# Optimization experiments

Hardware: AMD Instinct MI355X
Metric: run time of the kernel (lower is better)

Reference implementation:

```python
import jax, jax.numpy as jnp
import numpy as np

N_NODES = 100000
IN_DIM = 64
HID = 128
HID2 = HID // 2
N_CLASSES = 2
N_EDGES = 1600000
BN_EPS = 1e-5


def setup_inputs() -> dict:
    key = jax.random.key(0)
    ks = jax.random.split(key, 12)
    x = jax.random.normal(ks[0], (N_NODES, IN_DIM), dtype=jnp.float32)
    edge_index = jax.random.randint(ks[1], (2, N_EDGES), 0, N_NODES, dtype=jnp.int64)
    s = lambda k, shp, fan: jax.random.normal(k, shp, dtype=jnp.float32) / np.sqrt(fan)
    return {
        "x": x,
        "edge_index": edge_index,
        # SAGEConv1: lin_l (on aggregated neighbors, has bias), lin_r (root, no bias)
        "W1_l": s(ks[2], (IN_DIM, HID), IN_DIM),
        "b1_l": jnp.zeros((HID,), jnp.float32),
        "W1_r": s(ks[3], (IN_DIM, HID), IN_DIM),
        # SAGEConv2
        "W2_l": s(ks[4], (HID, HID2), HID),
        "b2_l": jnp.zeros((HID2,), jnp.float32),
        "W2_r": s(ks[5], (HID, HID2), HID),
        # BatchNorm (eval mode: running stats)
        "bn1_gamma": jnp.ones((HID,), jnp.float32),
        "bn1_beta": jnp.zeros((HID,), jnp.float32),
        "bn1_mean": jax.random.normal(ks[6], (HID,), dtype=jnp.float32) * 0.1,
        "bn1_var": jax.random.uniform(ks[7], (HID,), minval=0.5, maxval=1.5, dtype=jnp.float32),
        "bn2_gamma": jnp.ones((HID2,), jnp.float32),
        "bn2_beta": jnp.zeros((HID2,), jnp.float32),
        "bn2_mean": jax.random.normal(ks[8], (HID2,), dtype=jnp.float32) * 0.1,
        "bn2_var": jax.random.uniform(ks[9], (HID2,), minval=0.5, maxval=1.5, dtype=jnp.float32),
        # classifier
        "Wc": s(ks[10], (HID2, N_CLASSES), HID2),
        "bc": jnp.zeros((N_CLASSES,), jnp.float32),
    }


def _sage_mean(h, src, dst, Wl, bl, Wr, n_nodes):
    # gather source-node features along edges, scatter-mean into destinations
    msg = h[src]                                            # [E, D]
    summed = jax.ops.segment_sum(msg, dst, num_segments=n_nodes)  # [N, D]
    cnt = jax.ops.segment_sum(jnp.ones_like(dst, dtype=h.dtype), dst, num_segments=n_nodes)
    mean = summed / jnp.maximum(cnt, 1.0)[:, None]
    return mean @ Wl + bl + h @ Wr


def _bn_eval(h, gamma, beta, mean, var):
    return (h - mean) * (gamma * jax.lax.rsqrt(var + BN_EPS)) + beta


def reference(x, edge_index, W1_l, b1_l, W1_r, W2_l, b2_l, W2_r,
              bn1_gamma, bn1_beta, bn1_mean, bn1_var,
              bn2_gamma, bn2_beta, bn2_mean, bn2_var, Wc, bc):
    src, dst = edge_index[0], edge_index[1]
    n = x.shape[0]
    h = _sage_mean(x, src, dst, W1_l, b1_l, W1_r, n)
    h = jax.nn.relu(_bn_eval(h, bn1_gamma, bn1_beta, bn1_mean, bn1_var))
    h = _sage_mean(h, src, dst, W2_l, b2_l, W2_r, n)
    h = jax.nn.relu(_bn_eval(h, bn2_gamma, bn2_beta, bn2_mean, bn2_var))
    return h @ Wc + bc  # logits [N, num_classes]
```

## Files before the change

### kernel.cpp

```cpp
#include <hip/hip_runtime.h>
#include <math.h>

#define N_NODES 100000
#define IN_DIM 64
#define HID 128
#define HID2 64
#define N_EDGES 1600000
#define BN_EPS 1e-5f

#define NPB 128
#define NB 782
#define BIN_BLOCKS 391
#define BIN_CHUNK 4096
#define SORT_CAP 4096
#define CAST_BLOCKS 6250

typedef __attribute__((ext_vector_type(8))) __bf16 bf16x8;
typedef __attribute__((ext_vector_type(4))) float f32x4;
typedef __attribute__((ext_vector_type(2))) float f32x2;
typedef __attribute__((ext_vector_type(8))) unsigned short u16x8;

__device__ __forceinline__ unsigned short f2bf(float f) {
    unsigned int u = __builtin_bit_cast(unsigned int, f);
    u += 0x7fffu + ((u >> 16) & 1u);
    return (unsigned short)(u >> 16);
}

__device__ __forceinline__ void accum_fp8x8(float a[8], uint2 v) {
    f32x2 p0 = __builtin_amdgcn_cvt_pk_f32_fp8((int)v.x, false);
    f32x2 p1 = __builtin_amdgcn_cvt_pk_f32_fp8((int)v.x, true);
    f32x2 p2 = __builtin_amdgcn_cvt_pk_f32_fp8((int)v.y, false);
    f32x2 p3 = __builtin_amdgcn_cvt_pk_f32_fp8((int)v.y, true);
    a[0] += p0.x; a[1] += p0.y; a[2] += p1.x; a[3] += p1.y;
    a[4] += p2.x; a[5] += p2.y; a[6] += p3.x; a[7] += p3.y;
}

__device__ __forceinline__ void accum_fp8x16(float a[16], uint4 v) {
    unsigned int w[4] = {v.x, v.y, v.z, v.w};
    #pragma unroll
    for (int k = 0; k < 4; ++k) {
        f32x2 lo = __builtin_amdgcn_cvt_pk_f32_fp8((int)w[k], false);
        f32x2 hi = __builtin_amdgcn_cvt_pk_f32_fp8((int)w[k], true);
        a[4*k+0] += lo.x; a[4*k+1] += lo.y;
        a[4*k+2] += hi.x; a[4*k+3] += hi.y;
    }
}

__global__ __launch_bounds__(256) void prep_all(
    const float* __restrict__ x,
    const float* __restrict__ W1l, const float* __restrict__ W1r,
    const float* __restrict__ W2l, const float* __restrict__ W2r,
    unsigned short* __restrict__ Wf1, unsigned short* __restrict__ Wf2,
    unsigned short* __restrict__ xbf,
    unsigned char* __restrict__ x8,
    int* __restrict__ bucketTotal)
{
    const int bid = blockIdx.x;
    if (bid < 16) {
        int task = bid * 4 + (threadIdx.x >> 6);
        int lane = threadIdx.x & 63;
        int m  = task >> 5;
        int nt = (task >> 2) & 7;
        int kt = task & 3;
        int col = nt * 16 + (lane & 15);
        int k0  = kt * 32 + (lane >> 4) * 8;
        unsigned short tmp[8];
        #pragma unroll
        for (int e = 0; e < 8; ++e) {
            int k = k0 + e;
            float v;
            if (m == 0) v = (k < 64) ? W1l[k * HID + col] : W1r[(k - 64) * HID + col];
            else        v = (col < 64) ? W2l[k * HID2 + col] : W2r[k * HID2 + (col - 64)];
            tmp[e] = f2bf(v);
        }
        unsigned short* dst = ((m == 0) ? Wf1 : Wf2)
                            + ((size_t)((nt * 4 + kt) * 64 + lane)) * 8;
        *(u16x8*)dst = *(const u16x8*)tmp;
    } else if (bid < 16 + CAST_BLOCKS) {
        int tid = (bid - 16) * 256 + threadIdx.x;
        int node = tid >> 4;
        int q    = tid & 15;
        float4 v = ((const float4*)x)[tid];
        unsigned short o[4] = {f2bf(v.x), f2bf(v.y), f2bf(v.z), f2bf(v.w)};
        *(uint2*)(xbf + (size_t)node * 64 + q * 4) = *(const uint2*)o;
        int p = __builtin_amdgcn_cvt_pk_fp8_f32(v.x, v.y, 0, false);
        p     = __builtin_amdgcn_cvt_pk_fp8_f32(v.z, v.w, p, true);
        *(unsigned int*)(x8 + (size_t)node * 64 + q * 4) = (unsigned int)p;
    } else {
        for (int i = threadIdx.x; i < NB; i += 256) bucketTotal[i] = 0;
    }
}

__global__ __launch_bounds__(256) void bin_count(
    const int* __restrict__ dst,
    int* __restrict__ bucketTotal,
    int* __restrict__ perBlockBase)
{
    __shared__ int cnt[NB];
    const int t = threadIdx.x;
    for (int i = t; i < NB; i += 256) cnt[i] = 0;
    __syncthreads();
    const int e40 = blockIdx.x * (BIN_CHUNK / 4);
    const int4* dst4 = (const int4*)dst;
    #pragma unroll
    for (int i = 0; i < BIN_CHUNK / 4 / 256; ++i) {
        int ei = e40 + i * 256 + t;
        if (ei < N_EDGES / 4) {
            int4 d = dst4[ei];
            atomicAdd(&cnt[d.x >> 7], 1);
            atomicAdd(&cnt[d.y >> 7], 1);
            atomicAdd(&cnt[d.z >> 7], 1);
            atomicAdd(&cnt[d.w >> 7], 1);
        }
    }
    __syncthreads();
    for (int b = t; b < NB; b += 256) {
        int c = cnt[b];
        if (c) perBlockBase[blockIdx.x * NB + b] = atomicAdd(&bucketTotal[b], c);
    }
}

__global__ __launch_bounds__(1024) void bucket_scan(
    const int* __restrict__ bucketTotal, int* __restrict__ bucketStart)
{
    __shared__ int s[1024];
    const int t = threadIdx.x;
    int v = (t < NB) ? bucketTotal[t] : 0;
    s[t] = v;
    __syncthreads();
    #pragma unroll
    for (int off = 1; off < 1024; off <<= 1) {
        int u = (t >= off) ? s[t - off] : 0;
        __syncthreads();
        s[t] += u;
        __syncthreads();
    }
    if (t < NB) bucketStart[t] = s[t] - v;
    if (t == 0) bucketStart[NB] = N_EDGES;
}

__global__ __launch_bounds__(256) void bin_write(
    const int* __restrict__ src, const int* __restrict__ dst,
    const int* __restrict__ bucketStart,
    const int* __restrict__ perBlockBase,
    unsigned int* __restrict__ binned)
{
    __shared__ int cur[NB];
    const int t = threadIdx.x;
    for (int i = t; i < NB; i += 256) cur[i] = 0;
    __syncthreads();
    const int e40 = blockIdx.x * (BIN_CHUNK / 4);
    const int4* dst4 = (const int4*)dst;
    const int4* src4 = (const int4*)src;
    #pragma unroll
    for (int i = 0; i < BIN_CHUNK / 4 / 256; ++i) {
        int ei = e40 + i * 256 + t;
        if (ei < N_EDGES / 4) {
            int4 d = dst4[ei];
            int4 s = src4[ei];
            int ds[4] = {d.x, d.y, d.z, d.w};
            int ss[4] = {s.x, s.y, s.z, s.w};
            #pragma unroll
            for (int k = 0; k < 4; ++k) {
                int b = ds[k] >> 7;
                int pos = bucketStart[b] + perBlockBase[blockIdx.x * NB + b]
                        + atomicAdd(&cur[b], 1);
                binned[pos] = ((unsigned int)ss[k] << 7) | (unsigned int)(ds[k] & 127);
            }
        }
    }
}

__global__ __launch_bounds__(256) void bucket_sort(
    const unsigned int* __restrict__ binned,
    const int* __restrict__ bucketStart,
    int* __restrict__ sortedSrc,
    int* __restrict__ rowStart)
{
    __shared__ unsigned int stage[SORT_CAP];
    __shared__ int hist[NPB];
    __shared__ int cur[NPB];

    const int b  = blockIdx.x;
    const int t  = threadIdx.x;
    const int bs = bucketStart[b];
    const int be = bucketStart[b + 1];
    const int total = be - bs;

    if (t < NPB) hist[t] = 0;
    __syncthreads();

    if (total <= SORT_CAP) {
        for (int i = t; i < total; i += 256) {
            unsigned int p = binned[bs + i];
            stage[i] = p;
            atomicAdd(&hist[p & 127], 1);
        }
        __syncthreads();
        int orig = (t < NPB) ? hist[t] : 0;
        __syncthreads();
        #pragma unroll
        for (int off = 1; off < NPB; off <<= 1) {
            int v = (t < NPB && t >= off) ? hist[t - off] : 0;
            __syncthreads();
            if (t < NPB) hist[t] += v;
            __syncthreads();
        }
        if (t < NPB) {
            int excl = hist[t] - orig;
            int node = b * NPB + t;
            if (node < N_NODES) rowStart[node] = bs + excl;
            cur[t] = excl;
        }
        if (b == 0 && t == 0) rowStart[N_NODES] = N_EDGES;
        __syncthreads();
        for (int i = t; i < total; i += 256) {
            unsigned int p = stage[i];
            int pos = atomicAdd(&cur[p & 127], 1);
            sortedSrc[bs + pos] = (int)(p >> 7);
        }
    } else {
        for (int i = t; i < total; i += 256)
            atomicAdd(&hist[binned[bs + i] & 127], 1);
        __syncthreads();
        int orig = (t < NPB) ? hist[t] : 0;
        __syncthreads();
        #pragma unroll
        for (int off = 1; off < NPB; off <<= 1) {
            int v = (t < NPB && t >= off) ? hist[t - off] : 0;
            __syncthreads();
            if (t < NPB) hist[t] += v;
            __syncthreads();
        }
        if (t < NPB) {
            int excl = hist[t] - orig;
            int node = b * NPB + t;
            if (node < N_NODES) rowStart[node] = bs + excl;
            cur[t] = excl;
        }
        if (b == 0 && t == 0) rowStart[N_NODES] = N_EDGES;
        __syncthreads();
        for (int i = t; i < total; i += 256) {
            unsigned int p = binned[bs + i];
            int pos = atomicAdd(&cur[p & 127], 1);
            sortedSrc[bs + pos] = (int)(p >> 7);
        }
    }
}

__global__ __launch_bounds__(256, 4) void gemm_fused_g(
    const int* __restrict__ rowStart,
    const int* __restrict__ sortedSrc,
    const unsigned char* __restrict__ x8,
    const unsigned short* __restrict__ xbf,
    const unsigned short* __restrict__ Wf1,
    const unsigned short* __restrict__ Wf2,
    const float* __restrict__ b1l,
    const float* __restrict__ g1, const float* __restrict__ be1,
    const float* __restrict__ m1, const float* __restrict__ v1,
    const float* __restrict__ b2l,
    unsigned char* __restrict__ t1f8,
    unsigned short* __restrict__ r1bf)
{
    __shared__ unsigned short Al[64 * 136];

    const int t = threadIdx.x;
    const int w = t >> 6, l = t & 63;
    const int n0 = blockIdx.x * 64;
    const int r   = t >> 2;
    const int sub = t & 3;
    const int gb  = l & 60;
    const int node = n0 + r;

    {
        unsigned short* drow = &Al[r * 136 + 64 + sub * 16];
        if (node < N_NODES) {
            const uint4* sp = (const uint4*)(xbf + (size_t)node * 64 + sub * 16);
            uint4 v0 = sp[0], v1 = sp[1];
            *(uint4*)drow = v0;
            *(uint4*)(drow + 8) = v1;
        } else {
            uint4 z; z.x = z.y = z.z = z.w = 0u;
            *(uint4*)drow = z;
            *(uint4*)(drow + 8) = z;
        }
    }

    {
        unsigned short* drow = &Al[r * 136 + sub * 16];
        if (node < N_NODES) {
            const int b = rowStart[node], e = rowStart[node + 1];
            float a[16] = {};
            for (int base = b; base < e; base += 4) {
                const int cnt = min(e - base, 4);
                int srcv = (base + sub < e) ? sortedSrc[base + sub] : 0;
                if (cnt == 4) {
                    int s0 = __shfl(srcv, gb + 0);
                    int s1 = __shfl(srcv, gb + 1);
                    int s2 = __shfl(srcv, gb + 2);
                    int s3 = __shfl(srcv, gb + 3);
                    uint4 v0 = *(const uint4*)(x8 + (size_t)s0 * 64 + sub * 16);
                    uint4 v1 = *(const uint4*)(x8 + (size_t)s1 * 64 + sub * 16);
                    uint4 v2 = *(const uint4*)(x8 + (size_t)s2 * 64 + sub * 16);
                    uint4 v3 = *(const uint4*)(x8 + (size_t)s3 * 64 + sub * 16);
                    accum_fp8x16(a, v0);
                    accum_fp8x16(a, v1);
                    accum_fp8x16(a, v2);
                    accum_fp8x16(a, v3);
                } else {
                    for (int i = 0; i < cnt; ++i) {
                        int s0 = __shfl(srcv, gb + i);
                        uint4 v0 = *(const uint4*)(x8 + (size_t)s0 * 64 + sub * 16);
                        accum_fp8x16(a, v0);
                    }
                }
            }
            float inv = 1.0f / fmaxf((float)(e - b), 1.0f);
            unsigned short o[16];
            #pragma unroll
            for (int i = 0; i < 16; ++i) o[i] = f2bf(a[i] * inv);
            *(uint4*)drow       = *(const uint4*)o;
            *(uint4*)(drow + 8) = *(const uint4*)(o + 8);
        } else {
            uint4 z; z.x = z.y = z.z = z.w = 0u;
            *(uint4*)drow = z;
            *(uint4*)(drow + 8) = z;
        }
    }
    __syncthreads();

    const int row = l & 15, kq = l >> 4;

    f32x4 acc[4][2];
    #pragma unroll
    for (int a = 0; a < 4; ++a)
        #pragma unroll
        for (int b = 0; b < 2; ++b) acc[a][b] = (f32x4)(0.0f);

    #pragma unroll
    for (int kt = 0; kt < 4; ++kt) {
        bf16x8 bfr[2];
        #pragma unroll
        for (int n = 0; n < 2; ++n)
            bfr[n] = __builtin_bit_cast(bf16x8,
                *(const u16x8*)(Wf1 + ((size_t)(((2 * w + n) * 4 + kt) * 64 + l)) * 8));
        #pragma unroll
        for (int mt = 0; mt < 4; ++mt) {
            bf16x8 afr = __builtin_bit_cast(bf16x8,
                *(const u16x8*)&Al[(mt * 16 + row) * 136 + kt * 32 + kq * 8]);
            #pragma unroll
            for (int n = 0; n < 2; ++n)
                acc[mt][n] = __builtin_amdgcn_mfma_f32_16x16x32_bf16(
                    afr, bfr[n], acc[mt][n], 0, 0, 0);
        }
    }
    __syncthreads();

    #pragma unroll
    for (int n = 0; n < 2; ++n) {
        int j = w * 32 + n * 16 + (l & 15);
        float s  = g1[j] * rsqrtf(v1[j] + BN_EPS);
        float of = be1[j] + (b1l[j] - m1[j]) * s;
        #pragma unroll
        for (int mt = 0; mt < 4; ++mt) {
            #pragma unroll
            for (int i = 0; i < 4; ++i) {
                float h = fmaxf(fmaf(acc[mt][n][i], s, of), 0.0f);
                Al[(mt * 16 + kq * 4 + i) * 136 + j] = f2bf(h);
            }
        }
    }
    __syncthreads();

    f32x4 acc2[4][2];
    #pragma unroll
    for (int a = 0; a < 4; ++a)
        #pragma unroll
        for (int b = 0; b < 2; ++b) acc2[a][b] = (f32x4)(0.0f);

    #pragma unroll
    for (int kt = 0; kt < 4; ++kt) {
        bf16x8 bfr[2];
        #pragma unroll
        for (int n = 0; n < 2; ++n)
            bfr[n] = __builtin_bit_cast(bf16x8,
                *(const u16x8*)(Wf2 + ((size_t)(((2 * w + n) * 4 + kt) * 64 + l)) * 8));
        #pragma unroll
        for (int mt = 0; mt < 4; ++mt) {
            bf16x8 afr = __builtin_bit_cast(bf16x8,
                *(const u16x8*)&Al[(mt * 16 + row) * 136 + kt * 32 + kq * 8]);
            #pragma unroll
            for (int n = 0; n < 2; ++n)
                acc2[mt][n] = __builtin_amdgcn_mfma_f32_16x16x32_bf16(
                    afr, bfr[n], acc2[mt][n], 0, 0, 0);
        }
    }

    #pragma unroll
    for (int n = 0; n < 2; ++n) {
        int j = w * 32 + n * 16 + (l & 15);
        float bl = (w >= 2) ? b2l[j - 64] : 0.0f;
        #pragma unroll
        for (int mt = 0; mt < 4; ++mt) {
            #pragma unroll
            for (int i = 0; i < 4; ++i) {
                int nn = n0 + mt * 16 + kq * 4 + i;
                if (nn < N_NODES) {
                    float vv = acc2[mt][n][i];
                    if (w < 2) {
                        int p = __builtin_amdgcn_cvt_pk_fp8_f32(vv, vv, 0, false);
                        t1f8[(size_t)nn * 64 + j] = (unsigned char)(p & 0xff);
                    } else {
                        r1bf[(size_t)nn * 64 + (j - 64)] = f2bf(vv + bl);
                    }
                }
            }
        }
    }
}

__global__ __launch_bounds__(256) void gather2_e(
    const unsigned char* __restrict__ t1f8,
    const int* __restrict__ rowStart,
    const int* __restrict__ sortedSrc,
    const unsigned short* __restrict__ r1bf,
    const float* __restrict__ g2, const float* __restrict__ be2,
    const float* __restrict__ m2, const float* __restrict__ v2,
    const float* __restrict__ Wc, const float* __restrict__ bc,
    float* __restrict__ out)
{
    const int node = (int)((blockIdx.x * 256u + threadIdx.x) >> 3);
    const int lane = threadIdx.x & 63;
    const int f    = lane & 7;
    const int nb   = lane & 56;
    const int b = rowStart[node], e = rowStart[node + 1];

    float a0[8] = {}, a1[8] = {}, a2[8] = {}, a3[8] = {};

    for (int base = b; base < e; base += 8) {
        const int cnt = min(e - base, 8);
        int srcv = (base + f < e) ? sortedSrc[base + f] : 0;
        int i = 0;
        for (; i + 4 <= cnt; i += 4) {
            int s0 = __shfl(srcv, nb + i);
            int s1 = __shfl(srcv, nb + i + 1);
            int s2 = __shfl(srcv, nb + i + 2);
            int s3 = __shfl(srcv, nb + i + 3);
            accum_fp8x8(a0, *(const uint2*)(t1f8 + (size_t)s0 * 64 + f * 8));
            accum_fp8x8(a1, *(const uint2*)(t1f8 + (size_t)s1 * 64 + f * 8));
            accum_fp8x8(a2, *(const uint2*)(t1f8 + (size_t)s2 * 64 + f * 8));
            accum_fp8x8(a3, *(const uint2*)(t1f8 + (size_t)s3 * 64 + f * 8));
        }
        for (; i < cnt; ++i) {
            int s0 = __shfl(srcv, nb + i);
            accum_fp8x8(a0, *(const uint2*)(t1f8 + (size_t)s0 * 64 + f * 8));
        }
    }
    #pragma unroll
    for (int i = 0; i < 8; ++i) a0[i] = (a0[i] + a1[i]) + (a2[i] + a3[i]);

    const float inv = 1.0f / fmaxf((float)(e - b), 1.0f);
    const int f0 = f * 8;
    uint4 rv = *(const uint4*)(r1bf + (size_t)node * 64 + f0);
    unsigned int rw[4] = {rv.x, rv.y, rv.z, rv.w};
    float l0 = 0.f, l1 = 0.f;
    #pragma unroll
    for (int i = 0; i < 8; ++i) {
        int fe = f0 + i;
        unsigned int wv = rw[i >> 1];
        float rr = (i & 1) ? __builtin_bit_cast(float, wv)
                           : __builtin_bit_cast(float, wv << 16);
        float pre = a0[i] * inv + rr;
        float s   = g2[fe] * rsqrtf(v2[fe] + BN_EPS);
        float h2  = fmaxf((pre - m2[fe]) * s + be2[fe], 0.0f);
        l0 = fmaf(h2, Wc[fe * 2 + 0], l0);
        l1 = fmaf(h2, Wc[fe * 2 + 1], l1);
    }
    #pragma unroll
    for (int off = 4; off > 0; off >>= 1) {
        l0 += __shfl_xor(l0, off);
        l1 += __shfl_xor(l1, off);
    }
    if (f == 0) {
        out[(size_t)node * 2 + 0] = l0 + bc[0];
        out[(size_t)node * 2 + 1] = l1 + bc[1];
    }
}

extern "C" void kernel_launch(void* const* d_in, const int* in_sizes, int n_in,
                              void* d_out, int out_size, void* d_ws, size_t ws_size,
                              hipStream_t stream)
{
    const float* x    = (const float*)d_in[0];
    const int*   eidx = (const int*)d_in[1];
    const float* W1l  = (const float*)d_in[2];
    const float* b1l  = (const float*)d_in[3];
    const float* W1r  = (const float*)d_in[4];
    const float* W2l  = (const float*)d_in[5];
    const float* b2l  = (const float*)d_in[6];
    const float* W2r  = (const float*)d_in[7];
    const float* g1   = (const float*)d_in[8];
    const float* be1  = (const float*)d_in[9];
    const float* m1   = (const float*)d_in[10];
    const float* v1   = (const float*)d_in[11];
    const float* g2   = (const float*)d_in[12];
    const float* be2  = (const float*)d_in[13];
    const float* m2   = (const float*)d_in[14];
    const float* v2   = (const float*)d_in[15];
    const float* Wc   = (const float*)d_in[16];
    const float* bc   = (const float*)d_in[17];
    float* out = (float*)d_out;

    const int* src = eidx;
    const int* dst = eidx + N_EDGES;

    char* ws = (char*)d_ws;
    size_t off = 0;
    auto alloc = [&](size_t bytes) { void* p = ws + off; off = (off + bytes + 255) & ~(size_t)255; return p; };
    int* bucketTotal  = (int*)alloc((size_t)NB * 4);
    int* bucketStart  = (int*)alloc((size_t)(NB + 1) * 4);
    int* perBlockBase = (int*)alloc((size_t)BIN_BLOCKS * NB * 4);
    unsigned int* binned = (unsigned int*)alloc((size_t)N_EDGES * 4);
    int* sortedSrc    = (int*)alloc((size_t)N_EDGES * 4);
    int* rowStart     = (int*)alloc((size_t)(N_NODES + 1) * 4);
    unsigned short* Wf1  = (unsigned short*)alloc(128 * 128 * 2);
    unsigned short* Wf2  = (unsigned short*)alloc(128 * 128 * 2);
    unsigned short* xbf  = (unsigned short*)alloc((size_t)N_NODES * 64 * 2);
    unsigned char*  x8   = (unsigned char*)alloc((size_t)N_NODES * 64);
    unsigned char*  t1f8 = (unsigned char*)alloc((size_t)N_NODES * 64);
    unsigned short* r1bf = (unsigned short*)alloc((size_t)N_NODES * 64 * 2);

    const int gemmGrid    = (N_NODES + 63) / 64;
    const int gatherGrid  = (N_NODES * 8) / 256;

    prep_all<<<16 + CAST_BLOCKS + 1, 256, 0, stream>>>(
        x, W1l, W1r, W2l, W2r, Wf1, Wf2, xbf, x8, bucketTotal);

    bin_count  <<<BIN_BLOCKS, 256, 0, stream>>>(dst, bucketTotal, perBlockBase);
    bucket_scan<<<1, 1024, 0, stream>>>(bucketTotal, bucketStart);
    bin_write  <<<BIN_BLOCKS, 256, 0, stream>>>(src, dst, bucketStart, perBlockBase, binned);
    bucket_sort<<<NB, 256, 0, stream>>>(binned, bucketStart, sortedSrc, rowStart);

    gemm_fused_g<<<gemmGrid, 256, 0, stream>>>(
        rowStart, sortedSrc, x8, xbf, Wf1, Wf2,
        b1l, g1, be1, m1, v1, b2l, t1f8, r1bf);

    gather2_e<<<gatherGrid, 256, 0, stream>>>(
        t1f8, rowStart, sortedSrc, r1bf, g2, be2, m2, v2, Wc, bc, out);
}
```

Before: 135.6 us.

## Fuse bin counting into prep kernel, shrink bin chunks, unroll gather by eight

Moves the per-block destination histogram into the prep_all launch as extra blocks, so one kernel launch disappears. bucketTotal is now zeroed by a memset issued ahead of that launch. The bin chunk drops to 1024 edges, giving four times as many blocks for more parallelism, at the cost of a larger perBlockBase array and more global atomics. The second-layer gather now issues all eight neighbour loads before accumulating, to keep more memory requests in flight.

Measured after the change: 175.1 us. 29.1% more time.

```diff
diff --git a/kernel.cpp b/kernel.cpp
--- a/kernel.cpp
+++ b/kernel.cpp
@@ -10,8 +10,8 @@
 
 #define NPB 128
 #define NB 782
-#define BIN_BLOCKS 391
-#define BIN_CHUNK 4096
+#define BIN_BLOCKS 1563
+#define BIN_CHUNK 1024
 #define SORT_CAP 4096
 #define CAST_BLOCKS 6250
 
@@ -50,15 +50,18 @@
     const float* __restrict__ x,
     const float* __restrict__ W1l, const float* __restrict__ W1r,
     const float* __restrict__ W2l, const float* __restrict__ W2r,
+    const int* __restrict__ dst,
     unsigned short* __restrict__ Wf1, unsigned short* __restrict__ Wf2,
     unsigned short* __restrict__ xbf,
     unsigned char* __restrict__ x8,
-    int* __restrict__ bucketTotal)
+    int* __restrict__ bucketTotal,
+    int* __restrict__ perBlockBase)
 {
     const int bid = blockIdx.x;
+    const int t = threadIdx.x;
     if (bid < 16) {
-        int task = bid * 4 + (threadIdx.x >> 6);
-        int lane = threadIdx.x & 63;
+        int task = bid * 4 + (t >> 6);
+        int lane = t & 63;
         int m  = task >> 5;
         int nt = (task >> 2) & 7;
         int kt = task & 3;
@@ -73,11 +76,11 @@
             else        v = (col < 64) ? W2l[k * HID2 + col] : W2r[k * HID2 + (col - 64)];
             tmp[e] = f2bf(v);
         }
-        unsigned short* dst = ((m == 0) ? Wf1 : Wf2)
-                            + ((size_t)((nt * 4 + kt) * 64 + lane)) * 8;
-        *(u16x8*)dst = *(const u16x8*)tmp;
+        unsigned short* dstp = ((m == 0) ? Wf1 : Wf2)
+                             + ((size_t)((nt * 4 + kt) * 64 + lane)) * 8;
+        *(u16x8*)dstp = *(const u16x8*)tmp;
     } else if (bid < 16 + CAST_BLOCKS) {
-        int tid = (bid - 16) * 256 + threadIdx.x;
+        int tid = (bid - 16) * 256 + t;
         int node = tid >> 4;
         int q    = tid & 15;
         float4 v = ((const float4*)x)[tid];
@@ -87,36 +90,23 @@
         p     = __builtin_amdgcn_cvt_pk_fp8_f32(v.z, v.w, p, true);
         *(unsigned int*)(x8 + (size_t)node * 64 + q * 4) = (unsigned int)p;
     } else {
-        for (int i = threadIdx.x; i < NB; i += 256) bucketTotal[i] = 0;
-    }
-}
-
-__global__ __launch_bounds__(256) void bin_count(
-    const int* __restrict__ dst,
-    int* __restrict__ bucketTotal,
-    int* __restrict__ perBlockBase)
-{
-    __shared__ int cnt[NB];
-    const int t = threadIdx.x;
-    for (int i = t; i < NB; i += 256) cnt[i] = 0;
-    __syncthreads();
-    const int e40 = blockIdx.x * (BIN_CHUNK / 4);
-    const int4* dst4 = (const int4*)dst;
-    #pragma unroll
-    for (int i = 0; i < BIN_CHUNK / 4 / 256; ++i) {
-        int ei = e40 + i * 256 + t;
+        __shared__ int cnt[NB];
+        const int b2 = bid - (16 + CAST_BLOCKS);
+        for (int i = t; i < NB; i += 256) cnt[i] = 0;
+        __syncthreads();
+        int ei = b2 * (BIN_CHUNK / 4) + t;
         if (ei < N_EDGES / 4) {
-            int4 d = dst4[ei];
+            int4 d = ((const int4*)dst)[ei];
             atomicAdd(&cnt[d.x >> 7], 1);
             atomicAdd(&cnt[d.y >> 7], 1);
             atomicAdd(&cnt[d.z >> 7], 1);
             atomicAdd(&cnt[d.w >> 7], 1);
         }
-    }
-    __syncthreads();
-    for (int b = t; b < NB; b += 256) {
-        int c = cnt[b];
-        if (c) perBlockBase[blockIdx.x * NB + b] = atomicAdd(&bucketTotal[b], c);
+        __syncthreads();
+        for (int b = t; b < NB; b += 256) {
+            int c = cnt[b];
+            if (c) perBlockBase[b2 * NB + b] = atomicAdd(&bucketTotal[b], c);
+        }
     }
 }
 
@@ -149,24 +139,18 @@
     const int t = threadIdx.x;
     for (int i = t; i < NB; i += 256) cur[i] = 0;
     __syncthreads();
-    const int e40 = blockIdx.x * (BIN_CHUNK / 4);
-    const int4* dst4 = (const int4*)dst;
-    const int4* src4 = (const int4*)src;
-    #pragma unroll
-    for (int i = 0; i < BIN_CHUNK / 4 / 256; ++i) {
-        int ei = e40 + i * 256 + t;
-        if (ei < N_EDGES / 4) {
-            int4 d = dst4[ei];
-            int4 s = src4[ei];
-            int ds[4] = {d.x, d.y, d.z, d.w};
-            int ss[4] = {s.x, s.y, s.z, s.w};
-            #pragma unroll
-            for (int k = 0; k < 4; ++k) {
-                int b = ds[k] >> 7;
-                int pos = bucketStart[b] + perBlockBase[blockIdx.x * NB + b]
-                        + atomicAdd(&cur[b], 1);
-                binned[pos] = ((unsigned int)ss[k] << 7) | (unsigned int)(ds[k] & 127);
-            }
+    int ei = blockIdx.x * (BIN_CHUNK / 4) + t;
+    if (ei < N_EDGES / 4) {
+        int4 d = ((const int4*)dst)[ei];
+        int4 s = ((const int4*)src)[ei];
+        int ds[4] = {d.x, d.y, d.z, d.w};
+        int ss[4] = {s.x, s.y, s.z, s.w};
+        #pragma unroll
+        for (int k = 0; k < 4; ++k) {
+            int b = ds[k] >> 7;
+            int pos = bucketStart[b] + perBlockBase[blockIdx.x * NB + b]
+                    + atomicAdd(&cur[b], 1);
+            binned[pos] = ((unsigned int)ss[k] << 7) | (unsigned int)(ds[k] & 127);
         }
     }
 }
@@ -440,20 +424,36 @@
     for (int base = b; base < e; base += 8) {
         const int cnt = min(e - base, 8);
         int srcv = (base + f < e) ? sortedSrc[base + f] : 0;
-        int i = 0;
-        for (; i + 4 <= cnt; i += 4) {
-            int s0 = __shfl(srcv, nb + i);
-            int s1 = __shfl(srcv, nb + i + 1);
-            int s2 = __shfl(srcv, nb + i + 2);
-            int s3 = __shfl(srcv, nb + i + 3);
-            accum_fp8x8(a0, *(const uint2*)(t1f8 + (size_t)s0 * 64 + f * 8));
-            accum_fp8x8(a1, *(const uint2*)(t1f8 + (size_t)s1 * 64 + f * 8));
-            accum_fp8x8(a2, *(const uint2*)(t1f8 + (size_t)s2 * 64 + f * 8));
-            accum_fp8x8(a3, *(const uint2*)(t1f8 + (size_t)s3 * 64 + f * 8));
-        }
-        for (; i < cnt; ++i) {
-            int s0 = __shfl(srcv, nb + i);
-            accum_fp8x8(a0, *(const uint2*)(t1f8 + (size_t)s0 * 64 + f * 8));
+        if (cnt == 8) {
+            int s0 = __shfl(srcv, nb + 0);
+            int s1 = __shfl(srcv, nb + 1);
+            int s2 = __shfl(srcv, nb + 2);
+            int s3 = __shfl(srcv, nb + 3);
+            int s4 = __shfl(srcv, nb + 4);
+            int s5 = __shfl(srcv, nb + 5);
+            int s6 = __shfl(srcv, nb + 6);
+            int s7 = __shfl(srcv, nb + 7);
+            uint2 v0 = *(const uint2*)(t1f8 + (size_t)s0 * 64 + f * 8);
+            uint2 v1 = *(const uint2*)(t1f8 + (size_t)s1 * 64 + f * 8);
+            uint2 v2 = *(const uint2*)(t1f8 + (size_t)s2 * 64 + f * 8);
+            uint2 v3 = *(const uint2*)(t1f8 + (size_t)s3 * 64 + f * 8);
+            uint2 v4 = *(const uint2*)(t1f8 + (size_t)s4 * 64 + f * 8);
+            uint2 v5 = *(const uint2*)(t1f8 + (size_t)s5 * 64 + f * 8);
+            uint2 v6 = *(const uint2*)(t1f8 + (size_t)s6 * 64 + f * 8);
+            uint2 v7 = *(const uint2*)(t1f8 + (size_t)s7 * 64 + f * 8);
+            accum_fp8x8(a0, v0);
+            accum_fp8x8(a1, v1);
+            accum_fp8x8(a2, v2);
+            accum_fp8x8(a3, v3);
+            accum_fp8x8(a0, v4);
+            accum_fp8x8(a1, v5);
+            accum_fp8x8(a2, v6);
+            accum_fp8x8(a3, v7);
+        } else {
+            for (int i = 0; i < cnt; ++i) {
+                int s0 = __shfl(srcv, nb + i);
+                accum_fp8x8(a0, *(const uint2*)(t1f8 + (size_t)s0 * 64 + f * 8));
+            }
         }
     }
     #pragma unroll
@@ -533,10 +533,10 @@
     const int gemmGrid    = (N_NODES + 63) / 64;
     const int gatherGrid  = (N_NODES * 8) / 256;
 
-    prep_all<<<16 + CAST_BLOCKS + 1, 256, 0, stream>>>(
-        x, W1l, W1r, W2l, W2r, Wf1, Wf2, xbf, x8, bucketTotal);
-
-    bin_count  <<<BIN_BLOCKS, 256, 0, stream>>>(dst, bucketTotal, perBlockBase);
+    hipMemsetAsync(bucketTotal, 0, (size_t)NB * 4, stream);
+    prep_all<<<16 + CAST_BLOCKS + BIN_BLOCKS, 256, 0, stream>>>(
+        x, W1l, W1r, W2l, W2r, dst, Wf1, Wf2, xbf, x8, bucketTotal, perBlockBase);
+
     bucket_scan<<<1, 1024, 0, stream>>>(bucketTotal, bucketStart);
     bin_write  <<<BIN_BLOCKS, 256, 0, stream>>>(src, dst, bucketStart, perBlockBase, binned);
     bucket_sort<<<NB, 256, 0, stream>>>(binned, bucketStart, sortedSrc, rowStart);
```
